# Optimization experiments

Measured on AMD Instinct MI355X. Metric: run time of the kernel, lower is better.

Reference implementation:

```python
import jax, jax.numpy as jnp
import numpy as np

NUM_USERS = 100000
NUM_ITEMS = 50000
D = 64            # args.recdim
N_LAYERS = 3      # args.layer
NNZ = 4800000     # edges in the normalized bipartite adjacency (COO)
N = NUM_USERS + NUM_ITEMS


def setup_inputs() -> dict:
    key = jax.random.key(0)
    k1, k2, k3, k4, k5 = jax.random.split(key, 5)
    # LightGCN inits embeddings with normal(std=0.1)
    user_emb = 0.1 * jax.random.normal(k1, (NUM_USERS, D), dtype=jnp.float32)
    item_emb = 0.1 * jax.random.normal(k2, (NUM_ITEMS, D), dtype=jnp.float32)
    adj_rows = jax.random.randint(k3, (NNZ,), 0, N)
    adj_cols = jax.random.randint(k4, (NNZ,), 0, N)
    # stand-in for D^{-1/2} A D^{-1/2} normalized values
    adj_vals = jax.random.uniform(k5, (NNZ,), dtype=jnp.float32)
    return {"user_emb": user_emb, "item_emb": item_emb,
            "adj_vals": adj_vals, "adj_rows": adj_rows, "adj_cols": adj_cols}


def _spmm(rows, cols, vals, x, n):
    # sparse [n,n] @ dense [n,d] via gather + segment-sum (COO SpMM)
    return jax.ops.segment_sum(vals[:, None] * x[cols], rows, num_segments=n)


def reference(user_emb, item_emb, adj_vals, adj_rows, adj_cols):
    n_users = user_emb.shape[0]
    n = n_users + item_emb.shape[0]
    all_emb = jnp.concatenate([user_emb, item_emb], axis=0)  # [N, D]
    embs = [all_emb]
    for _ in range(N_LAYERS):  # fixed small hop count
        all_emb = _spmm(adj_rows, adj_cols, adj_vals, all_emb, n)
        embs.append(all_emb)
    light_out = jnp.mean(jnp.stack(embs, axis=1), axis=1)  # [N, D]
    users = light_out[:n_users]
    items = light_out[n_users:]
    return users, items
```

## Files before the change

kernel.cpp:

```cpp
#include <hip/hip_runtime.h>


#define NUSERS 100000
#define NITEMS 50000
#define NTOT   150000
#define DIM    64
#define NNZ_E  4800000

#define RPB     512
#define RSH     9
#define NBUCK   ((NTOT + RPB - 1) / RPB)
#define CHUNK_E 8192
#define NPART   ((NNZ_E + CHUNK_E - 1) / CHUNK_E)

__device__ __forceinline__ unsigned short benc(float f) {
    union { float f; unsigned u; } t; t.f = f;
    unsigned r = t.u + 0x7FFFu + ((t.u >> 16) & 1u);
    return (unsigned short)(r >> 16);
}
__device__ __forceinline__ float blo(unsigned g) { return __uint_as_float(g << 16); }
__device__ __forceinline__ float bhi(unsigned g) { return __uint_as_float(g & 0xFFFF0000u); }

__global__ void zero_int(int* __restrict__ p, int n) {
    int i = blockIdx.x * blockDim.x + threadIdx.x;
    if (i < n) p[i] = 0;
}

__global__ void histb_kernel(const int* __restrict__ rows, int* __restrict__ cnt) {
    __shared__ int l[NBUCK];
    for (int k = threadIdx.x; k < NBUCK; k += blockDim.x) l[k] = 0;
    __syncthreads();
    int stride = gridDim.x * blockDim.x;
    for (int e = blockIdx.x * blockDim.x + threadIdx.x; e < NNZ_E; e += stride)
        atomicAdd(&l[rows[e] >> RSH], 1);
    __syncthreads();
    for (int k = threadIdx.x; k < NBUCK; k += blockDim.x)
        if (l[k]) atomicAdd(&cnt[k], l[k]);
}

__global__ void scanb_kernel(const int* __restrict__ cnt, int* __restrict__ bptr,
                             int* __restrict__ gcur) {
    __shared__ int t[512];
    int tid = threadIdx.x;
    int v = (tid < NBUCK) ? cnt[tid] : 0;
    t[tid] = v;
    __syncthreads();
    for (int ofs = 1; ofs < 512; ofs <<= 1) {
        int a = (tid >= ofs) ? t[tid - ofs] : 0;
        __syncthreads();
        t[tid] += a;
        __syncthreads();
    }
    int excl = t[tid] - v;
    if (tid < NBUCK) { bptr[tid] = excl; gcur[tid] = excl; }
    if (tid == 511) bptr[NBUCK] = t[511];
}

__global__ void __launch_bounds__(512)
partA_kernel(const int* __restrict__ rows, const int* __restrict__ cols,
             const float* __restrict__ vals, int* __restrict__ gcur,
             int2* __restrict__ tmp) {
    __shared__ int l[NBUCK];
    int c0 = blockIdx.x * CHUNK_E;
    int c1 = c0 + CHUNK_E; if (c1 > NNZ_E) c1 = NNZ_E;
    for (int k = threadIdx.x; k < NBUCK; k += blockDim.x) l[k] = 0;
    __syncthreads();
    for (int e = c0 + threadIdx.x; e < c1; e += blockDim.x)
        atomicAdd(&l[rows[e] >> RSH], 1);
    __syncthreads();
    for (int k = threadIdx.x; k < NBUCK; k += blockDim.x) {
        int c = l[k];
        l[k] = c ? atomicAdd(&gcur[k], c) : 0;
    }
    __syncthreads();
    for (int e = c0 + threadIdx.x; e < c1; e += blockDim.x) {
        int r = rows[e];
        int b = r >> RSH, rl = r & (RPB - 1);
        int p = atomicAdd(&l[b], 1);
        tmp[p] = make_int2(cols[e] | (rl << 18), __float_as_int(vals[e]));
    }
}

__global__ void __launch_bounds__(1024)
partB_kernel(const int* __restrict__ bptr, const int2* __restrict__ tmp,
             unsigned* __restrict__ fin, int* __restrict__ rowptr) {
    __shared__ int cnt[RPB];
    __shared__ int cur[RPB];
    int b = blockIdx.x;
    int bb0 = bptr[b], bb1 = bptr[b + 1];
    int tid = threadIdx.x;
    if (tid < RPB) cnt[tid] = 0;
    __syncthreads();
    for (int e = bb0 + tid; e < bb1; e += 1024)
        atomicAdd(&cnt[((unsigned)tmp[e].x) >> 18], 1);
    __syncthreads();
    int v = 0;
    if (tid < RPB) { v = cnt[tid]; cur[tid] = v; }
    __syncthreads();
    for (int ofs = 1; ofs < RPB; ofs <<= 1) {
        int a = (tid < RPB && tid >= ofs) ? cur[tid - ofs] : 0;
        __syncthreads();
        if (tid < RPB) cur[tid] += a;
        __syncthreads();
    }
    if (tid < RPB) {
        int excl = cur[tid] - v;
        int row = b * RPB + tid;
        if (row < NTOT) rowptr[row] = bb0 + excl;
        cur[tid] = excl;
    }
    if (b == NBUCK - 1 && tid == 0) rowptr[NTOT] = bb1;
    __syncthreads();
    for (int e = bb0 + tid; e < bb1; e += 1024) {
        int2 t = tmp[e];
        int rl = ((unsigned)t.x) >> 18;
        int p = bb0 + atomicAdd(&cur[rl], 1);
        float val = __int_as_float(t.y);
        unsigned q = (unsigned)__float2int_rn(val * 16384.f);
        if (q > 16383u) q = 16383u;
        fin[p] = (((unsigned)t.x & 0x3FFFFu) << 14) | q;
    }
}

__global__ void convert_kernel(const float2* __restrict__ user, const float2* __restrict__ item,
                               unsigned* __restrict__ xh2) {
    int i = blockIdx.x * blockDim.x + threadIdx.x;
    if (i >= NTOT * 32) return;
    float2 v = (i < NUSERS * 32) ? user[i] : item[i - NUSERS * 32];
    xh2[i] = (unsigned)benc(v.x) | ((unsigned)benc(v.y) << 16);
}

__global__ void __launch_bounds__(256)
spmm_kernel(const int* __restrict__ rowptr, const unsigned* __restrict__ ed,
            const uint4* __restrict__ xin, uint4* __restrict__ yout,
            const float4* __restrict__ user, const float4* __restrict__ item,
            const uint4* __restrict__ y1, float4* __restrict__ out, int last) {
    int wid = blockIdx.x * (blockDim.x >> 6) + (threadIdx.x >> 6);
    int lane = threadIdx.x & 63;
    int oct = lane >> 3, s = lane & 7;
    int r = wid * 8 + oct;
    if (r >= NTOT) return;
    int start = rowptr[r];
    int end   = rowptr[r + 1];
    const float SCL = 1.f / 16384.f;
    float a0 = 0.f, a1 = 0.f, a2 = 0.f, a3 = 0.f, a4 = 0.f, a5 = 0.f, a6 = 0.f, a7 = 0.f;
    int i = start;
    for (; i + 8 <= end; i += 8) {
        unsigned e[8];
#pragma unroll
        for (int u = 0; u < 8; ++u) e[u] = ed[i + u];
        uint4 g[8];
#pragma unroll
        for (int u = 0; u < 8; ++u) g[u] = xin[(size_t)(e[u] >> 14) * 8 + s];
#pragma unroll
        for (int u = 0; u < 8; ++u) {
            float v = (float)(e[u] & 0x3FFFu) * SCL;
            a0 += v * blo(g[u].x); a1 += v * bhi(g[u].x);
            a2 += v * blo(g[u].y); a3 += v * bhi(g[u].y);
            a4 += v * blo(g[u].z); a5 += v * bhi(g[u].z);
            a6 += v * blo(g[u].w); a7 += v * bhi(g[u].w);
        }
    }
    for (; i < end; ++i) {
        unsigned e = ed[i];
        uint4 g = xin[(size_t)(e >> 14) * 8 + s];
        float v = (float)(e & 0x3FFFu) * SCL;
        a0 += v * blo(g.x); a1 += v * bhi(g.x);
        a2 += v * blo(g.y); a3 += v * bhi(g.y);
        a4 += v * blo(g.z); a5 += v * bhi(g.z);
        a6 += v * blo(g.w); a7 += v * bhi(g.w);
    }
    if (!last) {
        uint4 o;
        o.x = (unsigned)benc(a0) | ((unsigned)benc(a1) << 16);
        o.y = (unsigned)benc(a2) | ((unsigned)benc(a3) << 16);
        o.z = (unsigned)benc(a4) | ((unsigned)benc(a5) << 16);
        o.w = (unsigned)benc(a6) | ((unsigned)benc(a7) << 16);
        yout[(size_t)r * 8 + s] = o;
    } else {
        size_t f4 = (size_t)r * 16 + 2 * s;
        float4 x0a = (r < NUSERS) ? user[f4]     : item[f4     - (size_t)NUSERS * 16];
        float4 x0b = (r < NUSERS) ? user[f4 + 1] : item[f4 + 1 - (size_t)NUSERS * 16];
        uint4 u1 = y1[(size_t)r * 8 + s];
        uint4 u2 = xin[(size_t)r * 8 + s];
        float4 oa, ob;
        oa.x = 0.25f * (x0a.x + blo(u1.x) + blo(u2.x) + a0);
        oa.y = 0.25f * (x0a.y + bhi(u1.x) + bhi(u2.x) + a1);
        oa.z = 0.25f * (x0a.z + blo(u1.y) + blo(u2.y) + a2);
        oa.w = 0.25f * (x0a.w + bhi(u1.y) + bhi(u2.y) + a3);
        ob.x = 0.25f * (x0b.x + blo(u1.z) + blo(u2.z) + a4);
        ob.y = 0.25f * (x0b.y + bhi(u1.z) + bhi(u2.z) + a5);
        ob.z = 0.25f * (x0b.z + blo(u1.w) + blo(u2.w) + a6);
        ob.w = 0.25f * (x0b.w + bhi(u1.w) + bhi(u2.w) + a7);
        out[f4]     = oa;
        out[f4 + 1] = ob;
    }
}

extern "C" void kernel_launch(void* const* d_in, const int* in_sizes, int n_in,
                              void* d_out, int out_size, void* d_ws, size_t ws_size,
                              hipStream_t stream) {
    const float* user = (const float*)d_in[0];
    const float* item = (const float*)d_in[1];
    const float* vals = (const float*)d_in[2];
    const int*   rows = (const int*)d_in[3];
    const int*   cols = (const int*)d_in[4];
    float* out = (float*)d_out;

    char* w = (char*)d_ws;
    int2*     tmp    = (int2*)w;     w += (size_t)NNZ_E * 8;
    unsigned* fin    = (unsigned*)w; w += (size_t)NNZ_E * 4;
    unsigned* bufA   = (unsigned*)w; w += (size_t)NTOT * DIM * 2;
    unsigned* bufB   = (unsigned*)w; w += (size_t)NTOT * DIM * 2;
    int*      rowptr = (int*)w;      w += (size_t)(NTOT + 1) * 4;
    int*      cnt    = (int*)w;      w += (size_t)NBUCK * 4;
    int*      bptr   = (int*)w;      w += (size_t)(NBUCK + 1) * 4;
    int*      gcur   = (int*)w;

    const int blk = 256;
    const int gConv = (NTOT * 32 + blk - 1) / blk;
    const int gSpmm = (NTOT / 8 + 3) / 4;

    zero_int<<<2, blk, 0, stream>>>(cnt, NBUCK);
    histb_kernel<<<1024, blk, 0, stream>>>(rows, cnt);
    scanb_kernel<<<1, 512, 0, stream>>>(cnt, bptr, gcur);
    partA_kernel<<<NPART, 512, 0, stream>>>(rows, cols, vals, gcur, tmp);
    partB_kernel<<<NBUCK, 1024, 0, stream>>>(bptr, tmp, fin, rowptr);

    convert_kernel<<<gConv, blk, 0, stream>>>((const float2*)user, (const float2*)item, bufA);

    spmm_kernel<<<gSpmm, blk, 0, stream>>>(rowptr, fin, (const uint4*)bufA, (uint4*)bufB,
                                           (const float4*)user, (const float4*)item,
                                           (const uint4*)bufB, (float4*)out, 0);
    spmm_kernel<<<gSpmm, blk, 0, stream>>>(rowptr, fin, (const uint4*)bufB, (uint4*)bufA,
                                           (const float4*)user, (const float4*)item,
                                           (const uint4*)bufB, (float4*)out, 0);
    spmm_kernel<<<gSpmm, blk, 0, stream>>>(rowptr, fin, (const uint4*)bufA, (uint4*)bufA,
                                           (const float4*)user, (const float4*)item,
                                           (const uint4*)bufB, (float4*)out, 1);
}
```

Baseline: 568.3 us.

## Replace global-atomic bucket partition with per-chunk count matrix scan and nontemporal streams

```diff
diff --git a/kernel.cpp b/kernel.cpp
--- a/kernel.cpp
+++ b/kernel.cpp
@@ -21,68 +21,73 @@
 __device__ __forceinline__ float blo(unsigned g) { return __uint_as_float(g << 16); }
 __device__ __forceinline__ float bhi(unsigned g) { return __uint_as_float(g & 0xFFFF0000u); }
 
-__global__ void zero_int(int* __restrict__ p, int n) {
-    int i = blockIdx.x * blockDim.x + threadIdx.x;
-    if (i < n) p[i] = 0;
-}
-
-__global__ void histb_kernel(const int* __restrict__ rows, int* __restrict__ cnt) {
-    __shared__ int l[NBUCK];
-    for (int k = threadIdx.x; k < NBUCK; k += blockDim.x) l[k] = 0;
-    __syncthreads();
-    int stride = gridDim.x * blockDim.x;
-    for (int e = blockIdx.x * blockDim.x + threadIdx.x; e < NNZ_E; e += stride)
-        atomicAdd(&l[rows[e] >> RSH], 1);
-    __syncthreads();
-    for (int k = threadIdx.x; k < NBUCK; k += blockDim.x)
-        if (l[k]) atomicAdd(&cnt[k], l[k]);
-}
-
-__global__ void scanb_kernel(const int* __restrict__ cnt, int* __restrict__ bptr,
-                             int* __restrict__ gcur) {
-    __shared__ int t[512];
-    int tid = threadIdx.x;
-    int v = (tid < NBUCK) ? cnt[tid] : 0;
-    t[tid] = v;
-    __syncthreads();
-    for (int ofs = 1; ofs < 512; ofs <<= 1) {
-        int a = (tid >= ofs) ? t[tid - ofs] : 0;
-        __syncthreads();
-        t[tid] += a;
-        __syncthreads();
-    }
-    int excl = t[tid] - v;
-    if (tid < NBUCK) { bptr[tid] = excl; gcur[tid] = excl; }
-    if (tid == 511) bptr[NBUCK] = t[511];
-}
-
 __global__ void __launch_bounds__(512)
-partA_kernel(const int* __restrict__ rows, const int* __restrict__ cols,
-             const float* __restrict__ vals, int* __restrict__ gcur,
-             int2* __restrict__ tmp) {
+partA1_kernel(const int* __restrict__ rows, int* __restrict__ cntmat) {
     __shared__ int l[NBUCK];
     int c0 = blockIdx.x * CHUNK_E;
     int c1 = c0 + CHUNK_E; if (c1 > NNZ_E) c1 = NNZ_E;
-    for (int k = threadIdx.x; k < NBUCK; k += blockDim.x) l[k] = 0;
-    __syncthreads();
-    for (int e = c0 + threadIdx.x; e < c1; e += blockDim.x)
+    for (int k = threadIdx.x; k < NBUCK; k += 512) l[k] = 0;
+    __syncthreads();
+    for (int e = c0 + threadIdx.x; e < c1; e += 512)
         atomicAdd(&l[rows[e] >> RSH], 1);
     __syncthreads();
-    for (int k = threadIdx.x; k < NBUCK; k += blockDim.x) {
-        int c = l[k];
-        l[k] = c ? atomicAdd(&gcur[k], c) : 0;
-    }
-    __syncthreads();
-    for (int e = c0 + threadIdx.x; e < c1; e += blockDim.x) {
+    int* dst = cntmat + (size_t)blockIdx.x * NBUCK;
+    for (int k = threadIdx.x; k < NBUCK; k += 512) dst[k] = l[k];
+}
+
+__global__ void colscanA_kernel(const int* __restrict__ cntmat, int* __restrict__ runoff,
+                                int* __restrict__ colTotal) {
+    int b = blockIdx.x * 64 + threadIdx.x;
+    if (b >= NBUCK) return;
+    int run = 0;
+#pragma unroll 4
+    for (int p = 0; p < NPART; ++p) {
+        int v = cntmat[(size_t)p * NBUCK + b];
+        runoff[(size_t)p * NBUCK + b] = run;
+        run += v;
+    }
+    colTotal[b] = run;
+}
+
+__global__ void colscanB_kernel(const int* __restrict__ colTotal, int* __restrict__ bptr) {
+    __shared__ int t[512];
+    int tid = threadIdx.x;
+    int v = (tid < NBUCK) ? colTotal[tid] : 0;
+    t[tid] = v;
+    __syncthreads();
+    for (int ofs = 1; ofs < 512; ofs <<= 1) {
+        int a = (tid >= ofs) ? t[tid - ofs] : 0;
+        __syncthreads();
+        t[tid] += a;
+        __syncthreads();
+    }
+    if (tid < NBUCK) bptr[tid] = t[tid] - v;
+    if (tid == 511) bptr[NBUCK] = t[511];
+}
+
+__global__ void __launch_bounds__(512)
+partA2_kernel(const int* __restrict__ rows, const int* __restrict__ cols,
+              const float* __restrict__ vals, const int* __restrict__ runoff,
+              const int* __restrict__ bptr, long long* __restrict__ tmp) {
+    __shared__ int cur[NBUCK];
+    int c0 = blockIdx.x * CHUNK_E;
+    int c1 = c0 + CHUNK_E; if (c1 > NNZ_E) c1 = NNZ_E;
+    const int* ro = runoff + (size_t)blockIdx.x * NBUCK;
+    for (int k = threadIdx.x; k < NBUCK; k += 512) cur[k] = bptr[k] + ro[k];
+    __syncthreads();
+    for (int e = c0 + threadIdx.x; e < c1; e += 512) {
         int r = rows[e];
         int b = r >> RSH, rl = r & (RPB - 1);
-        int p = atomicAdd(&l[b], 1);
-        tmp[p] = make_int2(cols[e] | (rl << 18), __float_as_int(vals[e]));
+        int p = atomicAdd(&cur[b], 1);
+        unsigned lo = (unsigned)cols[e] | ((unsigned)rl << 18);
+        unsigned hi = (unsigned)__float_as_int(vals[e]);
+        long long packed = (long long)(((unsigned long long)hi << 32) | lo);
+        __builtin_nontemporal_store(packed, &tmp[p]);
     }
 }
 
 __global__ void __launch_bounds__(1024)
-partB_kernel(const int* __restrict__ bptr, const int2* __restrict__ tmp,
+partB_kernel(const int* __restrict__ bptr, const long long* __restrict__ tmp,
              unsigned* __restrict__ fin, int* __restrict__ rowptr) {
     __shared__ int cnt[RPB];
     __shared__ int cur[RPB];
@@ -91,8 +96,10 @@
     int tid = threadIdx.x;
     if (tid < RPB) cnt[tid] = 0;
     __syncthreads();
-    for (int e = bb0 + tid; e < bb1; e += 1024)
-        atomicAdd(&cnt[((unsigned)tmp[e].x) >> 18], 1);
+    for (int e = bb0 + tid; e < bb1; e += 1024) {
+        unsigned lo = (unsigned)__builtin_nontemporal_load(&tmp[e]);
+        atomicAdd(&cnt[lo >> 18], 1);
+    }
     __syncthreads();
     int v = 0;
     if (tid < RPB) { v = cnt[tid]; cur[tid] = v; }
@@ -112,13 +119,15 @@
     if (b == NBUCK - 1 && tid == 0) rowptr[NTOT] = bb1;
     __syncthreads();
     for (int e = bb0 + tid; e < bb1; e += 1024) {
-        int2 t = tmp[e];
-        int rl = ((unsigned)t.x) >> 18;
+        long long t = __builtin_nontemporal_load(&tmp[e]);
+        unsigned lo = (unsigned)t;
+        unsigned hi = (unsigned)((unsigned long long)t >> 32);
+        int rl = lo >> 18;
         int p = bb0 + atomicAdd(&cur[rl], 1);
-        float val = __int_as_float(t.y);
+        float val = __uint_as_float(hi);
         unsigned q = (unsigned)__float2int_rn(val * 16384.f);
         if (q > 16383u) q = 16383u;
-        fin[p] = (((unsigned)t.x & 0x3FFFFu) << 14) | q;
+        __builtin_nontemporal_store(((lo & 0x3FFFFu) << 14) | q, &fin[p]);
     }
 }
 
@@ -148,7 +157,7 @@
     for (; i + 8 <= end; i += 8) {
         unsigned e[8];
 #pragma unroll
-        for (int u = 0; u < 8; ++u) e[u] = ed[i + u];
+        for (int u = 0; u < 8; ++u) e[u] = __builtin_nontemporal_load(&ed[i + u]);
         uint4 g[8];
 #pragma unroll
         for (int u = 0; u < 8; ++u) g[u] = xin[(size_t)(e[u] >> 14) * 8 + s];
@@ -162,7 +171,7 @@
         }
     }
     for (; i < end; ++i) {
-        unsigned e = ed[i];
+        unsigned e = __builtin_nontemporal_load(&ed[i]);
         uint4 g = xin[(size_t)(e >> 14) * 8 + s];
         float v = (float)(e & 0x3FFFu) * SCL;
         a0 += v * blo(g.x); a1 += v * bhi(g.x);
@@ -208,23 +217,25 @@
     float* out = (float*)d_out;
 
     char* w = (char*)d_ws;
-    int2*     tmp    = (int2*)w;     w += (size_t)NNZ_E * 8;
-    unsigned* fin    = (unsigned*)w; w += (size_t)NNZ_E * 4;
-    unsigned* bufA   = (unsigned*)w; w += (size_t)NTOT * DIM * 2;
-    unsigned* bufB   = (unsigned*)w; w += (size_t)NTOT * DIM * 2;
-    int*      rowptr = (int*)w;      w += (size_t)(NTOT + 1) * 4;
-    int*      cnt    = (int*)w;      w += (size_t)NBUCK * 4;
-    int*      bptr   = (int*)w;      w += (size_t)(NBUCK + 1) * 4;
-    int*      gcur   = (int*)w;
+    long long* tmp    = (long long*)w; w += (size_t)NNZ_E * 8;
+    unsigned*  fin    = (unsigned*)w;  w += (size_t)NNZ_E * 4;
+    unsigned*  bufA   = (unsigned*)w;  w += (size_t)NTOT * DIM * 2;
+    unsigned*  bufB   = (unsigned*)w;  w += (size_t)NTOT * DIM * 2;
+    int*       rowptr = (int*)w;       w += (size_t)(NTOT + 1) * 4;
+    int*       cntmat = (int*)w;       w += (size_t)NPART * NBUCK * 4;
+    int*       runoff = (int*)w;       w += (size_t)NPART * NBUCK * 4;
+    int*       colTotal = (int*)w;     w += (size_t)NBUCK * 4;
+    int*       bptr   = (int*)w;
 
     const int blk = 256;
     const int gConv = (NTOT * 32 + blk - 1) / blk;
     const int gSpmm = (NTOT / 8 + 3) / 4;
-
-    zero_int<<<2, blk, 0, stream>>>(cnt, NBUCK);
-    histb_kernel<<<1024, blk, 0, stream>>>(rows, cnt);
-    scanb_kernel<<<1, 512, 0, stream>>>(cnt, bptr, gcur);
-    partA_kernel<<<NPART, 512, 0, stream>>>(rows, cols, vals, gcur, tmp);
+    const int gCsA  = (NBUCK + 63) / 64;
+
+    partA1_kernel<<<NPART, 512, 0, stream>>>(rows, cntmat);
+    colscanA_kernel<<<gCsA, 64, 0, stream>>>(cntmat, runoff, colTotal);
+    colscanB_kernel<<<1, 512, 0, stream>>>(colTotal, bptr);
+    partA2_kernel<<<NPART, 512, 0, stream>>>(rows, cols, vals, runoff, bptr, tmp);
     partB_kernel<<<NBUCK, 1024, 0, stream>>>(bptr, tmp, fin, rowptr);
 
     convert_kernel<<<gConv, blk, 0, stream>>>((const float2*)user, (const float2*)item, bufA);
```

Result: slower. 866.7 us (+52.5%).

## Replace global atomic bucket reservation with per-chunk count matrix and column scans

Applied to the files above, without the earlier changes.

```diff
diff --git a/kernel.cpp b/kernel.cpp
--- a/kernel.cpp
+++ b/kernel.cpp
@@ -21,28 +21,44 @@
 __device__ __forceinline__ float blo(unsigned g) { return __uint_as_float(g << 16); }
 __device__ __forceinline__ float bhi(unsigned g) { return __uint_as_float(g & 0xFFFF0000u); }
 
-__global__ void zero_int(int* __restrict__ p, int n) {
-    int i = blockIdx.x * blockDim.x + threadIdx.x;
-    if (i < n) p[i] = 0;
-}
-
-__global__ void histb_kernel(const int* __restrict__ rows, int* __restrict__ cnt) {
+__global__ void __launch_bounds__(512)
+partA1_kernel(const int* __restrict__ rows, int* __restrict__ cntmatT) {
     __shared__ int l[NBUCK];
-    for (int k = threadIdx.x; k < NBUCK; k += blockDim.x) l[k] = 0;
-    __syncthreads();
-    int stride = gridDim.x * blockDim.x;
-    for (int e = blockIdx.x * blockDim.x + threadIdx.x; e < NNZ_E; e += stride)
+    int p = blockIdx.x;
+    int c0 = p * CHUNK_E;
+    int c1 = c0 + CHUNK_E; if (c1 > NNZ_E) c1 = NNZ_E;
+    for (int k = threadIdx.x; k < NBUCK; k += 512) l[k] = 0;
+    __syncthreads();
+    for (int e = c0 + threadIdx.x; e < c1; e += 512)
         atomicAdd(&l[rows[e] >> RSH], 1);
     __syncthreads();
-    for (int k = threadIdx.x; k < NBUCK; k += blockDim.x)
-        if (l[k]) atomicAdd(&cnt[k], l[k]);
-}
-
-__global__ void scanb_kernel(const int* __restrict__ cnt, int* __restrict__ bptr,
-                             int* __restrict__ gcur) {
+    for (int k = threadIdx.x; k < NBUCK; k += 512)
+        cntmatT[(size_t)k * NPART + p] = l[k];
+}
+
+__global__ void __launch_bounds__(1024)
+colscan1_kernel(const int* __restrict__ cntmatT, int* __restrict__ runoffT,
+                int* __restrict__ colTotal) {
+    __shared__ int t[1024];
+    int b = blockIdx.x;
+    int tid = threadIdx.x;
+    int v = (tid < NPART) ? cntmatT[(size_t)b * NPART + tid] : 0;
+    t[tid] = v;
+    __syncthreads();
+    for (int ofs = 1; ofs < 1024; ofs <<= 1) {
+        int a = (tid >= ofs) ? t[tid - ofs] : 0;
+        __syncthreads();
+        t[tid] += a;
+        __syncthreads();
+    }
+    if (tid < NPART) runoffT[(size_t)b * NPART + tid] = t[tid] - v;
+    if (tid == NPART - 1) colTotal[b] = t[tid];
+}
+
+__global__ void colscan2_kernel(const int* __restrict__ colTotal, int* __restrict__ bptr) {
     __shared__ int t[512];
     int tid = threadIdx.x;
-    int v = (tid < NBUCK) ? cnt[tid] : 0;
+    int v = (tid < NBUCK) ? colTotal[tid] : 0;
     t[tid] = v;
     __syncthreads();
     for (int ofs = 1; ofs < 512; ofs <<= 1) {
@@ -51,33 +67,26 @@
         t[tid] += a;
         __syncthreads();
     }
-    int excl = t[tid] - v;
-    if (tid < NBUCK) { bptr[tid] = excl; gcur[tid] = excl; }
+    if (tid < NBUCK) bptr[tid] = t[tid] - v;
     if (tid == 511) bptr[NBUCK] = t[511];
 }
 
 __global__ void __launch_bounds__(512)
-partA_kernel(const int* __restrict__ rows, const int* __restrict__ cols,
-             const float* __restrict__ vals, int* __restrict__ gcur,
-             int2* __restrict__ tmp) {
-    __shared__ int l[NBUCK];
-    int c0 = blockIdx.x * CHUNK_E;
+partA2_kernel(const int* __restrict__ rows, const int* __restrict__ cols,
+              const float* __restrict__ vals, const int* __restrict__ runoffT,
+              const int* __restrict__ bptr, int2* __restrict__ tmp) {
+    __shared__ int cur[NBUCK];
+    int p = blockIdx.x;
+    int c0 = p * CHUNK_E;
     int c1 = c0 + CHUNK_E; if (c1 > NNZ_E) c1 = NNZ_E;
-    for (int k = threadIdx.x; k < NBUCK; k += blockDim.x) l[k] = 0;
-    __syncthreads();
-    for (int e = c0 + threadIdx.x; e < c1; e += blockDim.x)
-        atomicAdd(&l[rows[e] >> RSH], 1);
-    __syncthreads();
-    for (int k = threadIdx.x; k < NBUCK; k += blockDim.x) {
-        int c = l[k];
-        l[k] = c ? atomicAdd(&gcur[k], c) : 0;
-    }
-    __syncthreads();
-    for (int e = c0 + threadIdx.x; e < c1; e += blockDim.x) {
+    for (int k = threadIdx.x; k < NBUCK; k += 512)
+        cur[k] = bptr[k] + runoffT[(size_t)k * NPART + p];
+    __syncthreads();
+    for (int e = c0 + threadIdx.x; e < c1; e += 512) {
         int r = rows[e];
         int b = r >> RSH, rl = r & (RPB - 1);
-        int p = atomicAdd(&l[b], 1);
-        tmp[p] = make_int2(cols[e] | (rl << 18), __float_as_int(vals[e]));
+        int q = atomicAdd(&cur[b], 1);
+        tmp[q] = make_int2(cols[e] | (rl << 18), __float_as_int(vals[e]));
     }
 }
 
@@ -114,11 +123,11 @@
     for (int e = bb0 + tid; e < bb1; e += 1024) {
         int2 t = tmp[e];
         int rl = ((unsigned)t.x) >> 18;
-        int p = bb0 + atomicAdd(&cur[rl], 1);
+        int q = bb0 + atomicAdd(&cur[rl], 1);
         float val = __int_as_float(t.y);
-        unsigned q = (unsigned)__float2int_rn(val * 16384.f);
-        if (q > 16383u) q = 16383u;
-        fin[p] = (((unsigned)t.x & 0x3FFFFu) << 14) | q;
+        unsigned qq = (unsigned)__float2int_rn(val * 16384.f);
+        if (qq > 16383u) qq = 16383u;
+        fin[q] = (((unsigned)t.x & 0x3FFFFu) << 14) | qq;
     }
 }
 
@@ -208,23 +217,24 @@
     float* out = (float*)d_out;
 
     char* w = (char*)d_ws;
-    int2*     tmp    = (int2*)w;     w += (size_t)NNZ_E * 8;
-    unsigned* fin    = (unsigned*)w; w += (size_t)NNZ_E * 4;
-    unsigned* bufA   = (unsigned*)w; w += (size_t)NTOT * DIM * 2;
-    unsigned* bufB   = (unsigned*)w; w += (size_t)NTOT * DIM * 2;
-    int*      rowptr = (int*)w;      w += (size_t)(NTOT + 1) * 4;
-    int*      cnt    = (int*)w;      w += (size_t)NBUCK * 4;
-    int*      bptr   = (int*)w;      w += (size_t)(NBUCK + 1) * 4;
-    int*      gcur   = (int*)w;
+    int2*     tmp      = (int2*)w;     w += (size_t)NNZ_E * 8;
+    unsigned* fin      = (unsigned*)w; w += (size_t)NNZ_E * 4;
+    unsigned* bufA     = (unsigned*)w; w += (size_t)NTOT * DIM * 2;
+    unsigned* bufB     = (unsigned*)w; w += (size_t)NTOT * DIM * 2;
+    int*      rowptr   = (int*)w;      w += (size_t)(NTOT + 1) * 4;
+    int*      cntmatT  = (int*)w;      w += (size_t)NPART * NBUCK * 4;
+    int*      runoffT  = (int*)w;      w += (size_t)NPART * NBUCK * 4;
+    int*      colTotal = (int*)w;      w += (size_t)NBUCK * 4;
+    int*      bptr     = (int*)w;
 
     const int blk = 256;
     const int gConv = (NTOT * 32 + blk - 1) / blk;
     const int gSpmm = (NTOT / 8 + 3) / 4;
 
-    zero_int<<<2, blk, 0, stream>>>(cnt, NBUCK);
-    histb_kernel<<<1024, blk, 0, stream>>>(rows, cnt);
-    scanb_kernel<<<1, 512, 0, stream>>>(cnt, bptr, gcur);
-    partA_kernel<<<NPART, 512, 0, stream>>>(rows, cols, vals, gcur, tmp);
+    partA1_kernel<<<NPART, 512, 0, stream>>>(rows, cntmatT);
+    colscan1_kernel<<<NBUCK, 1024, 0, stream>>>(cntmatT, runoffT, colTotal);
+    colscan2_kernel<<<1, 512, 0, stream>>>(colTotal, bptr);
+    partA2_kernel<<<NPART, 512, 0, stream>>>(rows, cols, vals, runoffT, bptr, tmp);
     partB_kernel<<<NBUCK, 1024, 0, stream>>>(bptr, tmp, fin, rowptr);
 
     convert_kernel<<<gConv, blk, 0, stream>>>((const float2*)user, (const float2*)item, bufA);
```

Result: faster. 531.3 us (-6.5%).
